# Kernel tuning notes

Hardware: AMD Instinct MI355X
Metric: run time of the kernel (lower is better)

The kernel has to match this reference:

```python
import jax, jax.numpy as jnp
import numpy as np

N = 1024      # num_nodes
D_IN = 2      # input_dim
H = 64        # num_units
K = 2         # diffusion_steps
E = 16        # embed_units
NUM_MX = 3 * K + 1  # 2 random-walk supports + 1 adaptive


def _random_walk_T(A):
    # calculate_random_walk_matrix(A).T = (D^-1 A).T
    d = A.sum(axis=1)
    d_inv = np.where(d > 0, 1.0 / d, 0.0).astype(np.float32)
    return (d_inv[:, None] * A).T.astype(np.float32)


def setup_inputs() -> dict:
    key = jax.random.key(0)
    ks = jax.random.split(key, 12)
    rng = np.random.default_rng(0)
    mask = rng.random((N, N)) < 0.02
    A = (mask * rng.random((N, N))).astype(np.float32)
    support0 = jnp.asarray(_random_walk_T(A))      # forward random walk
    support1 = jnp.asarray(_random_walk_T(A.T))    # backward random walk
    s = 0.05
    return {
        "inputs": jax.random.normal(ks[0], (64, N * D_IN), jnp.float32),
        "state": jax.random.normal(ks[1], (64, N * H), jnp.float32),
        "nodevec1": jax.random.normal(ks[2], (N, E), jnp.float32) * 0.1,
        "nodevec2": jax.random.normal(ks[3], (N, E), jnp.float32) * 0.1,
        "w1": jax.random.normal(ks[4], (E, E), jnp.float32) * 0.25,
        "b1": jnp.zeros((E,), jnp.float32),
        "w2": jax.random.normal(ks[5], (E, E), jnp.float32) * 0.25,
        "b2": jnp.zeros((E,), jnp.float32),
        "ru_wg": jax.random.normal(ks[6], (E, NUM_MX, D_IN + H, 2 * H), jnp.float32) * s,
        "ru_bg": jax.random.normal(ks[7], (E, 2 * H), jnp.float32) * s,
        "can_wg": jax.random.normal(ks[8], (E, NUM_MX, D_IN + H, H), jnp.float32) * s,
        "can_bg": jax.random.normal(ks[9], (E, H), jnp.float32) * s,
        "support0": support0,
        "support1": support1,
    }


def reference(inputs, state, nodevec1, nodevec2, w1, b1, w2, b2,
              ru_wg, ru_bg, can_wg, can_bg, support0, support1):
    B = inputs.shape[0]
    x_in = inputs.reshape(B, N, D_IN)
    h = state.reshape(B, N, H)

    # adaptive support: softmax(relu(E1 E2^T)) over last axis
    adp = jax.nn.softmax(jax.nn.relu(nodevec1 @ nodevec2.T), axis=-1)
    supports = [support0, support1, adp]

    # node-adaptive embedding: tanh(Dense(nodevec1)) * sigmoid(Dense(nodevec2))
    nv = jnp.tanh(nodevec1 @ w1 + b1) * jax.nn.sigmoid(nodevec2 @ w2 + b2)  # [N,E]

    def diff_conv(st, wg, bg):
        x0 = jnp.concatenate([x_in, st], axis=-1)  # [B,N,I], I = D_IN+H
        xs = [x0]
        for S in supports:  # Chebyshev-like recurrence per support
            p0 = x0
            p1 = jnp.einsum('nm,bmi->bni', S, x0)
            xs.append(p1)
            for _ in range(2, K + 1):
                p2 = 2.0 * jnp.einsum('nm,bmi->bni', S, p1) - p0
                xs.append(p2)
                p0, p1 = p1, p2
        x = jnp.stack(xs, axis=2)  # [B, N, NUM_MX, I]
        # per-node adaptive weights / bias
        w = jnp.einsum('nd,dkio->nkio', nv, wg)  # [N, NUM_MX, I, O]
        b = nv @ bg                              # [N, O]
        return jnp.einsum('bnki,nkio->bno', x, w) + b

    ru = jax.nn.sigmoid(diff_conv(h, ru_wg, ru_bg))    # [B,N,2H]
    r, u = jnp.split(ru, 2, axis=-1)
    c = jnp.tanh(diff_conv(r * h, can_wg, can_bg))     # [B,N,H]
    out = u * h + (1.0 - u) * c
    return out.reshape(B, N * H)
```

## Files before the change

### kernel.cpp

```cpp
#include <hip/hip_runtime.h>
#include <hip/hip_bf16.h>
#include <math.h>

#define NN 1024
#define BB 64
#define DIN 2
#define HH 64
#define II 66
#define EE 16
#define KMX 7
#define CC (BB*II)

typedef __attribute__((ext_vector_type(8))) short short8;
typedef __attribute__((ext_vector_type(4))) float f32x4;

__global__ __launch_bounds__(256) void k_adp_nv(
    const float* __restrict__ nv1, const float* __restrict__ nv2,
    const float* __restrict__ w1, const float* __restrict__ b1,
    const float* __restrict__ w2, const float* __restrict__ b2,
    __hip_bfloat16* __restrict__ adp_bf, float* __restrict__ nv)
{
  __shared__ float s_nv1[16];
  __shared__ float logits[1024];
  __shared__ float red[256];
  int n = blockIdx.x, t = threadIdx.x;
  if (t < 16) s_nv1[t] = nv1[n*16+t];
  __syncthreads();
  float lmax = -1e30f;
  for (int m = t; m < 1024; m += 256) {
    float acc = 0.f;
    const float* v2 = nv2 + m*16;
    #pragma unroll
    for (int d = 0; d < 16; ++d) acc += s_nv1[d]*v2[d];
    acc = fmaxf(acc, 0.f);
    logits[m] = acc;
    lmax = fmaxf(lmax, acc);
  }
  red[t] = lmax; __syncthreads();
  for (int s = 128; s > 0; s >>= 1) { if (t < s) red[t] = fmaxf(red[t], red[t+s]); __syncthreads(); }
  float mx = red[0]; __syncthreads();
  float lsum = 0.f;
  for (int m = t; m < 1024; m += 256) { float e = __expf(logits[m]-mx); logits[m] = e; lsum += e; }
  red[t] = lsum; __syncthreads();
  for (int s = 128; s > 0; s >>= 1) { if (t < s) red[t] += red[t+s]; __syncthreads(); }
  float inv = 1.f/red[0];
  for (int m = t; m < 1024; m += 256) adp_bf[n*1024+m] = __float2bfloat16(logits[m]*inv);
  if (t < 16) {
    float a = 0.f, c = 0.f;
    #pragma unroll
    for (int d = 0; d < 16; ++d) a += s_nv1[d]*w1[d*16+t];
    #pragma unroll
    for (int d = 0; d < 16; ++d) c += nv2[n*16+d]*w2[d*16+t];
    a = tanhf(a + b1[t]);
    c = 1.f/(1.f+expf(-(c + b2[t])));
    nv[n*16+t] = a*c;
  }
}

__global__ __launch_bounds__(256) void k_csr(
    const float* __restrict__ s0, const float* __restrict__ s1,
    float* __restrict__ vals, int* __restrict__ cols, int* __restrict__ cnts)
{
  int row = blockIdx.x & 1023;
  int sup = blockIdx.x >> 10;
  const float* S = (sup == 0) ? s0 : s1;
  __shared__ int cnt;
  if (threadIdx.x == 0) cnt = 0;
  __syncthreads();
  int base = (sup*1024 + row)*64;
  for (int m = threadIdx.x; m < 1024; m += 256) {
    float v = S[row*1024+m];
    if (v != 0.f) {
      int idx = atomicAdd(&cnt, 1);
      if (idx < 64) { cols[base+idx] = m; vals[base+idx] = v; }
    }
  }
  __syncthreads();
  if (threadIdx.x == 0) cnts[sup*1024+row] = min(cnt, 64);
}

template<int MODE>
__global__ __launch_bounds__(256) void k_x0(
    const float* __restrict__ inputs, const float* __restrict__ state,
    const float* __restrict__ ru, float* __restrict__ xs)
{
  int idx = blockIdx.x*256 + threadIdx.x;
  int i = idx % II;
  int b = (idx / II) % BB;
  int n = idx / (II*BB);
  float v;
  if (i < DIN) v = inputs[b*(NN*DIN) + n*DIN + i];
  else {
    v = state[b*(NN*HH) + n*HH + (i-DIN)];
    if (MODE == 1) v *= ru[(size_t)(n*BB + b)*128 + (i-DIN)];
  }
  xs[idx] = v;
}

template<int P2>
__global__ __launch_bounds__(256) void k_spmm(
    const float* __restrict__ vals, const int* __restrict__ cols, const int* __restrict__ cnts,
    int sup, const float* __restrict__ Xsrc, const float* __restrict__ X0, float* __restrict__ Y)
{
  int n = blockIdx.x;
  __shared__ float sv[64];
  __shared__ int sc[64];
  int cnt = cnts[sup*1024+n];
  if (threadIdx.x < 64 && threadIdx.x < cnt) {
    sv[threadIdx.x] = vals[(sup*1024+n)*64 + threadIdx.x];
    sc[threadIdx.x] = cols[(sup*1024+n)*64 + threadIdx.x] * (CC/4);
  }
  __syncthreads();
  const float4* X4  = (const float4*)Xsrc;
  const float4* X04 = (const float4*)X0;
  float4* Y4 = (float4*)Y;
  for (int c = threadIdx.x; c < CC/4; c += 256) {
    float4 acc = {0.f,0.f,0.f,0.f};
    for (int j = 0; j < cnt; ++j) {
      float s = sv[j];
      float4 x = X4[sc[j] + c];
      acc.x += s*x.x; acc.y += s*x.y; acc.z += s*x.z; acc.w += s*x.w;
    }
    size_t o = (size_t)n*(CC/4) + c;
    if (P2) {
      float4 z = X04[o];
      acc.x = 2.f*acc.x - z.x; acc.y = 2.f*acc.y - z.y;
      acc.z = 2.f*acc.z - z.z; acc.w = 2.f*acc.w - z.w;
    }
    Y4[o] = acc;
  }
}

__global__ __launch_bounds__(256) void k_xsplit(
    const float* __restrict__ in, __hip_bfloat16* __restrict__ out)
{
  __shared__ float t[64][65];
  int cb = blockIdx.x*64, kb = blockIdx.y*64;
  int tx = threadIdx.x & 63, ty = threadIdx.x >> 6;
  for (int r = ty; r < 64; r += 4) t[r][tx] = in[(size_t)(kb+r)*CC + cb+tx];
  __syncthreads();
  int kp = threadIdx.x & 31, cr0 = threadIdx.x >> 5;
  for (int cr = cr0; cr < 64; cr += 8) {
    __hip_bfloat16 h0 = __float2bfloat16(t[kp*2][cr]);
    __hip_bfloat16 h1 = __float2bfloat16(t[kp*2+1][cr]);
    ushort2 u;
    u.x = *(unsigned short*)&h0;
    u.y = *(unsigned short*)&h1;
    *(ushort2*)&out[(size_t)(cb+cr)*1024 + kb + kp*2] = u;
  }
}

template<int P2>
__global__ __launch_bounds__(64) void k_gemm_mfma(
    const __hip_bfloat16* __restrict__ A, const __hip_bfloat16* __restrict__ XT,
    const float* __restrict__ X0, float* __restrict__ Y)
{
  int l = threadIdx.x;
  int c0 = blockIdx.x*64, m0 = blockIdx.y*64;
  int lr = l & 15, lg = l >> 4;
  f32x4 acc[4][4] = {};
  const short* Ab  = (const short*)A;
  const short* Xb  = (const short*)XT;
  for (int k0 = 0; k0 < 1024; k0 += 32) {
    short8 af[4], bf[4];
    #pragma unroll
    for (int mf = 0; mf < 4; ++mf)
      af[mf] = *(const short8*)&Ab[(size_t)(m0 + mf*16 + lr)*1024 + k0 + lg*8];
    #pragma unroll
    for (int cf = 0; cf < 4; ++cf)
      bf[cf] = *(const short8*)&Xb[(size_t)(c0 + cf*16 + lr)*1024 + k0 + lg*8];
    #pragma unroll
    for (int mf = 0; mf < 4; ++mf)
      #pragma unroll
      for (int cf = 0; cf < 4; ++cf)
        acc[mf][cf] = __builtin_amdgcn_mfma_f32_16x16x32_bf16(af[mf], bf[cf], acc[mf][cf], 0, 0, 0);
  }
  #pragma unroll
  for (int mf = 0; mf < 4; ++mf)
    #pragma unroll
    for (int cf = 0; cf < 4; ++cf)
      #pragma unroll
      for (int r = 0; r < 4; ++r) {
        int m = m0 + mf*16 + lg*4 + r;
        int c = c0 + cf*16 + lr;
        size_t o = (size_t)m*CC + c;
        float v = acc[mf][cf][r];
        Y[o] = P2 ? 2.f*v - X0[o] : v;
      }
}

template<int O>
__global__ __launch_bounds__(256) void k_genw(
    const float* __restrict__ nv, const float* __restrict__ wg,
    float* __restrict__ W, int n0)
{
  constexpr int KIO = KMX*II*O;
  __shared__ float snv[16][16];
  int t = threadIdx.x;
  int c0 = blockIdx.x * 1024;
  int nb = blockIdx.y * 16;
  snv[t >> 4][t & 15] = nv[(size_t)(n0 + nb + (t >> 4))*16 + (t & 15)];
  int e = c0 + t*4;
  bool ok = (e < KIO);
  f32x4 w[16];
  #pragma unroll
  for (int d = 0; d < 16; ++d) {
    if (ok) w[d] = *(const f32x4*)&wg[(size_t)d*KIO + e];
    else    w[d] = f32x4{0.f,0.f,0.f,0.f};
  }
  __syncthreads();
  #pragma unroll
  for (int node = 0; node < 16; ++node) {
    f32x4 a = {0.f,0.f,0.f,0.f};
    #pragma unroll
    for (int dq = 0; dq < 4; ++dq) {
      f32x4 s4 = *(const f32x4*)&snv[node][dq*4];
      a += s4.x * w[dq*4+0];
      a += s4.y * w[dq*4+1];
      a += s4.z * w[dq*4+2];
      a += s4.w * w[dq*4+3];
    }
    if (ok) *(f32x4*)&W[(size_t)(nb + node)*KIO + e] = a;
  }
}

template<int O, int ACT>
__global__ __launch_bounds__(256) void k_contract2(
    const float* __restrict__ xs, const float* __restrict__ W,
    const float* __restrict__ nv, const float* __restrict__ bg,
    float* __restrict__ outg, int n0)
{
  constexpr int G = O/64;
  __shared__ float xt[BB*II];
  __shared__ float Wt[II*O];
  __shared__ float snv[16];
  int n = n0 + blockIdx.x, t = threadIdx.x;
  if (t < 16) snv[t] = nv[n*16+t];
  int b0 = (t >> 4) * 4;
  int oc = (t & 15) * 4;
  float acc[4][G][4] = {};
  const float* Wn = W + (size_t)blockIdx.x*KMX*II*O;
  for (int k = 0; k < KMX; ++k) {
    __syncthreads();
    const float4* src = (const float4*)(xs + (size_t)(k*1024+n)*CC);
    for (int e = t; e < BB*II/4; e += 256) ((float4*)xt)[e] = src[e];
    const float4* wk = (const float4*)(Wn + (size_t)k*II*O);
    for (int e = t; e < II*O/4; e += 256) ((float4*)Wt)[e] = wk[e];
    __syncthreads();
    #pragma unroll 2
    for (int i = 0; i < II; ++i) {
      float xr[4];
      #pragma unroll
      for (int bb = 0; bb < 4; ++bb) xr[bb] = xt[(b0+bb)*II + i];
      #pragma unroll
      for (int g = 0; g < G; ++g) {
        float4 w4 = *(const float4*)&Wt[i*O + g*64 + oc];
        #pragma unroll
        for (int bb = 0; bb < 4; ++bb) {
          acc[bb][g][0] += xr[bb]*w4.x;
          acc[bb][g][1] += xr[bb]*w4.y;
          acc[bb][g][2] += xr[bb]*w4.z;
          acc[bb][g][3] += xr[bb]*w4.w;
        }
      }
    }
  }
  float bias[G][4];
  #pragma unroll
  for (int g = 0; g < G; ++g)
    #pragma unroll
    for (int q = 0; q < 4; ++q) {
      float bv = 0.f;
      #pragma unroll
      for (int d = 0; d < 16; ++d) bv += snv[d]*bg[d*O + g*64 + oc + q];
      bias[g][q] = bv;
    }
  #pragma unroll
  for (int bb = 0; bb < 4; ++bb) {
    float* dst = outg + (size_t)(n*BB + b0+bb)*O;
    #pragma unroll
    for (int g = 0; g < G; ++g) {
      float4 r;
      float v0 = acc[bb][g][0] + bias[g][0];
      float v1 = acc[bb][g][1] + bias[g][1];
      float v2 = acc[bb][g][2] + bias[g][2];
      float v3 = acc[bb][g][3] + bias[g][3];
      if (ACT) { r.x = tanhf(v0); r.y = tanhf(v1); r.z = tanhf(v2); r.w = tanhf(v3); }
      else {
        r.x = 1.f/(1.f+expf(-v0)); r.y = 1.f/(1.f+expf(-v1));
        r.z = 1.f/(1.f+expf(-v2)); r.w = 1.f/(1.f+expf(-v3));
      }
      *(float4*)&dst[g*64 + oc] = r;
    }
  }
}

template<int O, int ACT>
__global__ __launch_bounds__(256) void k_contract(
    const float* __restrict__ xs, const float* __restrict__ nv,
    const float* __restrict__ wg, const float* __restrict__ bg, float* __restrict__ outg)
{
  constexpr int G = O/64;
  __shared__ float xt[BB*II];
  __shared__ float Wt[II*O];
  __shared__ float snv[16];
  int n = blockIdx.x, t = threadIdx.x;
  if (t < 16) snv[t] = nv[n*16+t];
  int b0 = (t >> 4) * 4;
  int oc = (t & 15) * 4;
  float acc[4][G][4] = {};
  for (int k = 0; k < KMX; ++k) {
    __syncthreads();
    const float* src = xs + (size_t)(k*1024+n)*CC;
    for (int e = t; e < BB*II; e += 256) xt[e] = src[e];
    const float* wk = wg + (size_t)k*II*O;
    for (int e = t; e < II*O; e += 256) {
      float w = 0.f;
      #pragma unroll
      for (int d = 0; d < 16; ++d) w += snv[d]*wk[(size_t)d*KMX*II*O + e];
      Wt[e] = w;
    }
    __syncthreads();
    #pragma unroll 2
    for (int i = 0; i < II; ++i) {
      float xr[4];
      #pragma unroll
      for (int bb = 0; bb < 4; ++bb) xr[bb] = xt[(b0+bb)*II + i];
      #pragma unroll
      for (int g = 0; g < G; ++g) {
        float4 w4 = *(const float4*)&Wt[i*O + g*64 + oc];
        #pragma unroll
        for (int bb = 0; bb < 4; ++bb) {
          acc[bb][g][0] += xr[bb]*w4.x;
          acc[bb][g][1] += xr[bb]*w4.y;
          acc[bb][g][2] += xr[bb]*w4.z;
          acc[bb][g][3] += xr[bb]*w4.w;
        }
      }
    }
  }
  float bias[G][4];
  #pragma unroll
  for (int g = 0; g < G; ++g)
    #pragma unroll
    for (int q = 0; q < 4; ++q) {
      float bv = 0.f;
      #pragma unroll
      for (int d = 0; d < 16; ++d) bv += snv[d]*bg[d*O + g*64 + oc + q];
      bias[g][q] = bv;
    }
  #pragma unroll
  for (int bb = 0; bb < 4; ++bb) {
    float* dst = outg + (size_t)(n*BB + b0+bb)*O;
    #pragma unroll
    for (int g = 0; g < G; ++g) {
      float4 r;
      float v0 = acc[bb][g][0] + bias[g][0];
      float v1 = acc[bb][g][1] + bias[g][1];
      float v2 = acc[bb][g][2] + bias[g][2];
      float v3 = acc[bb][g][3] + bias[g][3];
      if (ACT) { r.x = tanhf(v0); r.y = tanhf(v1); r.z = tanhf(v2); r.w = tanhf(v3); }
      else {
        r.x = 1.f/(1.f+expf(-v0)); r.y = 1.f/(1.f+expf(-v1));
        r.z = 1.f/(1.f+expf(-v2)); r.w = 1.f/(1.f+expf(-v3));
      }
      *(float4*)&dst[g*64 + oc] = r;
    }
  }
}

__global__ __launch_bounds__(256) void k_out(
    const float* __restrict__ ru, const float* __restrict__ cb,
    const float* __restrict__ state, float* __restrict__ out)
{
  int idx = blockIdx.x*256 + threadIdx.x;
  int j = idx % HH;
  int b = (idx / HH) % BB;
  int n = idx / (HH*BB);
  float u = ru[(size_t)(n*BB+b)*128 + 64 + j];
  float h = state[(size_t)b*(NN*HH) + n*HH + j];
  float c = cb[(size_t)(n*BB+b)*HH + j];
  out[(size_t)b*(NN*HH) + n*HH + j] = u*h + (1.f-u)*c;
}

extern "C" void kernel_launch(void* const* d_in, const int* in_sizes, int n_in,
                              void* d_out, int out_size, void* d_ws, size_t ws_size,
                              hipStream_t stream)
{
  const float* inputs  = (const float*)d_in[0];
  const float* state   = (const float*)d_in[1];
  const float* nv1     = (const float*)d_in[2];
  const float* nv2     = (const float*)d_in[3];
  const float* w1      = (const float*)d_in[4];
  const float* b1      = (const float*)d_in[5];
  const float* w2      = (const float*)d_in[6];
  const float* b2      = (const float*)d_in[7];
  const float* ru_wg   = (const float*)d_in[8];
  const float* ru_bg   = (const float*)d_in[9];
  const float* can_wg  = (const float*)d_in[10];
  const float* can_bg  = (const float*)d_in[11];
  const float* support0= (const float*)d_in[12];
  const float* support1= (const float*)d_in[13];
  float* out = (float*)d_out;

  float* ws = (float*)d_ws;
  float* nv       = ws;
  float* csr_vals = nv + 16384;
  int*   csr_cols = (int*)(csr_vals + 131072);
  int*   csr_cnts = csr_cols + 131072;
  __hip_bfloat16* adp_bf = (__hip_bfloat16*)(csr_cnts + 2048);
  float* xs       = (float*)(csr_cnts + 2048) + 524288;
  float* ru       = xs + (size_t)KMX*NN*CC;
  float* cb       = ru + (size_t)NN*BB*128;
  __hip_bfloat16* XT = (__hip_bfloat16*)cb;
  float* Wbuf     = cb + (size_t)NN*BB*64;

  const size_t KIO128 = (size_t)KMX*II*128;
  size_t baseFloats = (size_t)(Wbuf - ws);
  size_t availFloats = (ws_size/4 > baseFloats) ? ws_size/4 - baseFloats : 0;
  int chunk = 0;
  if      (availFloats >= 1024*KIO128) chunk = 1024;
  else if (availFloats >=  512*KIO128) chunk = 512;
  else if (availFloats >=  256*KIO128) chunk = 256;
  else if (availFloats >=  128*KIO128) chunk = 128;
  else if (availFloats >=   64*KIO128) chunk = 64;

  k_adp_nv<<<1024, 256, 0, stream>>>(nv1, nv2, w1, b1, w2, b2, adp_bf, nv);
  k_csr<<<2048, 256, 0, stream>>>(support0, support1, csr_vals, csr_cols, csr_cnts);

  dim3 gxs(66, 16);
  dim3 ggm(66, 16);

  k_x0<0><<<16896, 256, 0, stream>>>(inputs, state, nullptr, xs);
  for (int s = 0; s < 2; ++s) {
    float* p1 = xs + (size_t)(1+2*s)*NN*CC;
    float* p2 = xs + (size_t)(2+2*s)*NN*CC;
    k_spmm<0><<<1024, 256, 0, stream>>>(csr_vals, csr_cols, csr_cnts, s, xs, nullptr, p1);
    k_spmm<1><<<1024, 256, 0, stream>>>(csr_vals, csr_cols, csr_cnts, s, p1, xs, p2);
  }
  {
    float* p1 = xs + (size_t)5*NN*CC;
    float* p2 = xs + (size_t)6*NN*CC;
    k_xsplit<<<gxs, 256, 0, stream>>>(xs, XT);
    k_gemm_mfma<0><<<ggm, 64, 0, stream>>>(adp_bf, XT, nullptr, p1);
    k_xsplit<<<gxs, 256, 0, stream>>>(p1, XT);
    k_gemm_mfma<1><<<ggm, 64, 0, stream>>>(adp_bf, XT, xs, p2);
  }
  if (chunk) {
    for (int n0 = 0; n0 < NN; n0 += chunk) {
      dim3 gg((KMX*II*128 + 1023)/1024, chunk/16);
      k_genw<128><<<gg, 256, 0, stream>>>(nv, ru_wg, Wbuf, n0);
      k_contract2<128,0><<<chunk, 256, 0, stream>>>(xs, Wbuf, nv, ru_bg, ru, n0);
    }
  } else {
    k_contract<128,0><<<1024, 256, 0, stream>>>(xs, nv, ru_wg, ru_bg, ru);
  }

  k_x0<1><<<16896, 256, 0, stream>>>(inputs, state, ru, xs);
  for (int s = 0; s < 2; ++s) {
    float* p1 = xs + (size_t)(1+2*s)*NN*CC;
    float* p2 = xs + (size_t)(2+2*s)*NN*CC;
    k_spmm<0><<<1024, 256, 0, stream>>>(csr_vals, csr_cols, csr_cnts, s, xs, nullptr, p1);
    k_spmm<1><<<1024, 256, 0, stream>>>(csr_vals, csr_cols, csr_cnts, s, p1, xs, p2);
  }
  {
    float* p1 = xs + (size_t)5*NN*CC;
    float* p2 = xs + (size_t)6*NN*CC;
    k_xsplit<<<gxs, 256, 0, stream>>>(xs, XT);
    k_gemm_mfma<0><<<ggm, 64, 0, stream>>>(adp_bf, XT, nullptr, p1);
    k_xsplit<<<gxs, 256, 0, stream>>>(p1, XT);
    k_gemm_mfma<1><<<ggm, 64, 0, stream>>>(adp_bf, XT, xs, p2);
  }
  if (chunk) {
    for (int n0 = 0; n0 < NN; n0 += chunk) {
      dim3 gg((KMX*II*64 + 1023)/1024, chunk/16);
      k_genw<64><<<gg, 256, 0, stream>>>(nv, can_wg, Wbuf, n0);
      k_contract2<64,1><<<chunk, 256, 0, stream>>>(xs, Wbuf, nv, can_bg, cb, n0);
    }
  } else {
    k_contract<64,1><<<1024, 256, 0, stream>>>(xs, nv, can_wg, can_bg, cb);
  }

  k_out<<<16384, 256, 0, stream>>>(ru, cb, state, out);
}
```

Measured before the change: 1.207 ms.

## Batch both supports in one SpMM launch and split contraction over output tiles

The two random-walk supports are now handled by a single SpMM launch per recurrence step, using blockIdx.y to pick the support, which halves the number of SpMM launches. The per-node contraction kernel is rebuilt to use 128-thread blocks that each compute a 32-column output slice, so the grid gets 4x (ru) or 2x (candidate) more blocks and each block needs less shared memory and fewer registers. The aim is more parallelism and occupancy in the contraction. The cost is that each output-group block reloads the full x tile for every support, which multiplies x reads from global memory.

```diff
diff --git a/kernel.cpp b/kernel.cpp
--- a/kernel.cpp
+++ b/kernel.cpp
@@ -98,11 +98,15 @@
 }
 
 template<int P2>
-__global__ __launch_bounds__(256) void k_spmm(
+__global__ __launch_bounds__(256) void k_spmm2(
     const float* __restrict__ vals, const int* __restrict__ cols, const int* __restrict__ cnts,
-    int sup, const float* __restrict__ Xsrc, const float* __restrict__ X0, float* __restrict__ Y)
+    float* __restrict__ xsb)
 {
   int n = blockIdx.x;
+  int sup = blockIdx.y;
+  const float* Xsrc = P2 ? xsb + (size_t)(1+2*sup)*NN*CC : xsb;
+  float* Y          = P2 ? xsb + (size_t)(2+2*sup)*NN*CC : xsb + (size_t)(1+2*sup)*NN*CC;
+  const float* X0   = xsb;
   __shared__ float sv[64];
   __shared__ int sc[64];
   int cnt = cnts[sup*1024+n];
@@ -225,73 +229,66 @@
 }
 
 template<int O, int ACT>
-__global__ __launch_bounds__(256) void k_contract2(
+__global__ __launch_bounds__(128) void k_contract3(
     const float* __restrict__ xs, const float* __restrict__ W,
     const float* __restrict__ nv, const float* __restrict__ bg,
     float* __restrict__ outg, int n0)
 {
-  constexpr int G = O/64;
   __shared__ float xt[BB*II];
-  __shared__ float Wt[II*O];
-  __shared__ float snv[16];
-  int n = n0 + blockIdx.x, t = threadIdx.x;
-  if (t < 16) snv[t] = nv[n*16+t];
-  int b0 = (t >> 4) * 4;
-  int oc = (t & 15) * 4;
-  float acc[4][G][4] = {};
-  const float* Wn = W + (size_t)blockIdx.x*KMX*II*O;
+  __shared__ float Wt[II*32];
+  int nb = blockIdx.x;
+  int og = blockIdx.y;
+  int n = n0 + nb;
+  int t = threadIdx.x;
+  int b0 = (t >> 3) * 4;
+  int oc = (t & 7) * 4;
+  float acc[4][4] = {};
   for (int k = 0; k < KMX; ++k) {
     __syncthreads();
     const float4* src = (const float4*)(xs + (size_t)(k*1024+n)*CC);
-    for (int e = t; e < BB*II/4; e += 256) ((float4*)xt)[e] = src[e];
-    const float4* wk = (const float4*)(Wn + (size_t)k*II*O);
-    for (int e = t; e < II*O/4; e += 256) ((float4*)Wt)[e] = wk[e];
+    for (int e = t; e < BB*II/4; e += 128) ((float4*)xt)[e] = src[e];
+    const float* wkb = W + ((size_t)nb*KMX + k)*II*O + og*32;
+    for (int e = t; e < II*8; e += 128) {
+      int i = e >> 3, c = (e & 7)*4;
+      *(float4*)&Wt[i*32 + c] = *(const float4*)&wkb[(size_t)i*O + c];
+    }
     __syncthreads();
     #pragma unroll 2
     for (int i = 0; i < II; ++i) {
+      float4 w4 = *(const float4*)&Wt[i*32 + oc];
       float xr[4];
       #pragma unroll
       for (int bb = 0; bb < 4; ++bb) xr[bb] = xt[(b0+bb)*II + i];
       #pragma unroll
-      for (int g = 0; g < G; ++g) {
-        float4 w4 = *(const float4*)&Wt[i*O + g*64 + oc];
-        #pragma unroll
-        for (int bb = 0; bb < 4; ++bb) {
-          acc[bb][g][0] += xr[bb]*w4.x;
-          acc[bb][g][1] += xr[bb]*w4.y;
-          acc[bb][g][2] += xr[bb]*w4.z;
-          acc[bb][g][3] += xr[bb]*w4.w;
-        }
+      for (int bb = 0; bb < 4; ++bb) {
+        acc[bb][0] += xr[bb]*w4.x;
+        acc[bb][1] += xr[bb]*w4.y;
+        acc[bb][2] += xr[bb]*w4.z;
+        acc[bb][3] += xr[bb]*w4.w;
       }
     }
   }
-  float bias[G][4];
-  #pragma unroll
-  for (int g = 0; g < G; ++g)
-    #pragma unroll
-    for (int q = 0; q < 4; ++q) {
-      float bv = 0.f;
-      #pragma unroll
-      for (int d = 0; d < 16; ++d) bv += snv[d]*bg[d*O + g*64 + oc + q];
-      bias[g][q] = bv;
-    }
+  float bias[4] = {0.f,0.f,0.f,0.f};
+  #pragma unroll
+  for (int d = 0; d < 16; ++d) {
+    float s = nv[(size_t)n*16 + d];
+    const float* bgr = bg + (size_t)d*O + og*32 + oc;
+    bias[0] += s*bgr[0]; bias[1] += s*bgr[1];
+    bias[2] += s*bgr[2]; bias[3] += s*bgr[3];
+  }
   #pragma unroll
   for (int bb = 0; bb < 4; ++bb) {
-    float* dst = outg + (size_t)(n*BB + b0+bb)*O;
-    #pragma unroll
-    for (int g = 0; g < G; ++g) {
-      float4 r;
-      float v0 = acc[bb][g][0] + bias[g][0];
-      float v1 = acc[bb][g][1] + bias[g][1];
-      float v2 = acc[bb][g][2] + bias[g][2];
-      float v3 = acc[bb][g][3] + bias[g][3];
-      if (ACT) { r.x = tanhf(v0); r.y = tanhf(v1); r.z = tanhf(v2); r.w = tanhf(v3); }
-      else {
-        r.x = 1.f/(1.f+expf(-v0)); r.y = 1.f/(1.f+expf(-v1));
-        r.z = 1.f/(1.f+expf(-v2)); r.w = 1.f/(1.f+expf(-v3));
-      }
-      *(float4*)&dst[g*64 + oc] = r;
-    }
+    float4 r;
+    float v0 = acc[bb][0] + bias[0];
+    float v1 = acc[bb][1] + bias[1];
+    float v2 = acc[bb][2] + bias[2];
+    float v3 = acc[bb][3] + bias[3];
+    if (ACT) { r.x = tanhf(v0); r.y = tanhf(v1); r.z = tanhf(v2); r.w = tanhf(v3); }
+    else {
+      r.x = 1.f/(1.f+expf(-v0)); r.y = 1.f/(1.f+expf(-v1));
+      r.z = 1.f/(1.f+expf(-v2)); r.w = 1.f/(1.f+expf(-v3));
+    }
+    *(float4*)&outg[(size_t)(n*BB + b0+bb)*O + og*32 + oc] = r;
   }
 }
 
@@ -430,14 +427,11 @@
 
   dim3 gxs(66, 16);
   dim3 ggm(66, 16);
+  dim3 gsp(1024, 2);
 
   k_x0<0><<<16896, 256, 0, stream>>>(inputs, state, nullptr, xs);
-  for (int s = 0; s < 2; ++s) {
-    float* p1 = xs + (size_t)(1+2*s)*NN*CC;
-    float* p2 = xs + (size_t)(2+2*s)*NN*CC;
-    k_spmm<0><<<1024, 256, 0, stream>>>(csr_vals, csr_cols, csr_cnts, s, xs, nullptr, p1);
-    k_spmm<1><<<1024, 256, 0, stream>>>(csr_vals, csr_cols, csr_cnts, s, p1, xs, p2);
-  }
+  k_spmm2<0><<<gsp, 256, 0, stream>>>(csr_vals, csr_cols, csr_cnts, xs);
+  k_spmm2<1><<<gsp, 256, 0, stream>>>(csr_vals, csr_cols, csr_cnts, xs);
   {
     float* p1 = xs + (size_t)5*NN*CC;
     float* p2 = xs + (size_t)6*NN*CC;
@@ -450,19 +444,16 @@
     for (int n0 = 0; n0 < NN; n0 += chunk) {
       dim3 gg((KMX*II*128 + 1023)/1024, chunk/16);
       k_genw<128><<<gg, 256, 0, stream>>>(nv, ru_wg, Wbuf, n0);
-      k_contract2<128,0><<<chunk, 256, 0, stream>>>(xs, Wbuf, nv, ru_bg, ru, n0);
+      dim3 gc(chunk, 4);
+      k_contract3<128,0><<<gc, 128, 0, stream>>>(xs, Wbuf, nv, ru_bg, ru, n0);
     }
   } else {
     k_contract<128,0><<<1024, 256, 0, stream>>>(xs, nv, ru_wg, ru_bg, ru);
   }
 
   k_x0<1><<<16896, 256, 0, stream>>>(inputs, state, ru, xs);
-  for (int s = 0; s < 2; ++s) {
-    float* p1 = xs + (size_t)(1+2*s)*NN*CC;
-    float* p2 = xs + (size_t)(2+2*s)*NN*CC;
-    k_spmm<0><<<1024, 256, 0, stream>>>(csr_vals, csr_cols, csr_cnts, s, xs, nullptr, p1);
-    k_spmm<1><<<1024, 256, 0, stream>>>(csr_vals, csr_cols, csr_cnts, s, p1, xs, p2);
-  }
+  k_spmm2<0><<<gsp, 256, 0, stream>>>(csr_vals, csr_cols, csr_cnts, xs);
+  k_spmm2<1><<<gsp, 256, 0, stream>>>(csr_vals, csr_cols, csr_cnts, xs);
   {
     float* p1 = xs + (size_t)5*NN*CC;
     float* p2 = xs + (size_t)6*NN*CC;
@@ -475,7 +466,8 @@
     for (int n0 = 0; n0 < NN; n0 += chunk) {
       dim3 gg((KMX*II*64 + 1023)/1024, chunk/16);
       k_genw<64><<<gg, 256, 0, stream>>>(nv, can_wg, Wbuf, n0);
-      k_contract2<64,1><<<chunk, 256, 0, stream>>>(xs, Wbuf, nv, can_bg, cb, n0);
+      dim3 gc(chunk, 2);
+      k_contract3<64,1><<<gc, 128, 0, stream>>>(xs, Wbuf, nv, can_bg, cb, n0);
     }
   } else {
     k_contract<64,1><<<1024, 256, 0, stream>>>(xs, nv, can_wg, can_bg, cb);
```

Measured after the change: 1.218 ms. Within noise of the previous version (+0.9%).
